# Kernel tuning notes

Hardware: AMD Instinct MI355X
Metric: run time of the kernel (lower is better)

The kernel has to match this reference:

```python
import jax, jax.numpy as jnp
import numpy as np

B, N, D = 128, 512, 128   # batch, nodes (= patch_len / time_window_size), feature dim (d_model_patch)
EPS = 1e-5                # torch BatchNorm1d default eps
SLOPE = 0.01              # torch F.leaky_relu default negative_slope
DIAG_INF = 1e8            # eyes_like * 100000000.0 in Dot_Graph_Construction_weights


def mask_matrix(T, decay):
    # Faithful replication of Mask_Matrix: slices i*T:(i+1)*T on a [T,T] array
    # are empty for i >= 1, so the result is all ones; we replicate exactly.
    A = np.ones((T, T), np.float32)
    for i in range(T):
        v = 0
        for r in range(i, T):
            A[i * T:(i + 1) * T, r * T:(r + 1) * T] *= decay ** v
            v += 1
        v = 0
        for r in range(i + 1):
            A[i * T:(i + 1) * T, (i - r) * T:(i - r + 1) * T] *= decay ** v
            v += 1
    return A


def setup_inputs() -> dict:
    key = jax.random.key(0)
    ks = jax.random.split(key, 3)
    s = 1.0 / np.sqrt(D)  # torch Linear default init scale
    return {
        "x": jax.random.normal(ks[0], (B, N, D), jnp.float32),
        "W_map": jax.random.uniform(ks[1], (D, D), jnp.float32, -s, s),
        "b_map": jnp.zeros((D,), jnp.float32),
        "W_theta": jax.random.uniform(ks[2], (D, D), jnp.float32, -s, s),
        "b_theta": jnp.zeros((D,), jnp.float32),
        "gamma_in": jnp.ones((D,), jnp.float32),
        "beta_in": jnp.zeros((D,), jnp.float32),
        "gamma_out": jnp.ones((D,), jnp.float32),
        "beta_out": jnp.zeros((D,), jnp.float32),
        "pre_relation": jnp.asarray(mask_matrix(N, 0.9)),
    }


def leaky_relu(x):
    return jnp.where(x >= 0, x, SLOPE * x)


def batchnorm(x, gamma, beta):
    # x: [B, N, C]; BatchNorm1d over channel C (training-mode batch stats,
    # matching torch transpose -> BN -> transpose pattern).
    mean = x.mean((0, 1))
    var = x.var((0, 1))
    return (x - mean) * jax.lax.rsqrt(var + EPS) * gamma + beta


def reference(x, W_map, b_map, W_theta, b_theta, gamma_in, beta_in,
              gamma_out, beta_out, pre_relation):
    # --- Dot_Graph_Construction_weights ---
    nf = x @ W_map + b_map                         # [B,N,D]
    adj = jnp.einsum('bnd,bmd->bnm', nf, nf)       # [B,N,N]
    eye = jnp.eye(N, dtype=x.dtype)
    adj = leaky_relu(adj - eye * DIAG_INF)
    adj = jax.nn.softmax(adj, axis=-1) + eye
    # --- decay mask (all-ones, computed faithfully) ---
    adj = adj * pre_relation
    # --- input BN ---
    xb = batchnorm(x, gamma_in, beta_in)
    # --- MPNN_mk_v2, k=1 ---
    h = jnp.einsum('bnm,bmd->bnd', adj, xb) @ W_theta + b_theta
    h = batchnorm(h, gamma_out, beta_out)
    return leaky_relu(h)                           # [B,N,D]
```

## Files before the change

### kernel.cpp

```cpp
#include <hip/hip_runtime.h>
#include <hip/hip_bf16.h>

#define B_ 128
#define N_ 512
#define D_ 128
#define M_ (B_ * N_)
#define LDSP 136

typedef unsigned short u16;
typedef short s8v __attribute__((ext_vector_type(8)));
typedef _Float16 h8v __attribute__((ext_vector_type(8)));
typedef __fp16 fp2v __attribute__((ext_vector_type(2)));
typedef float f4v __attribute__((ext_vector_type(4)));
typedef unsigned u4v __attribute__((ext_vector_type(4)));

__device__ __forceinline__ u16 f2h(float f) {
  _Float16 h = (_Float16)f;
  return __builtin_bit_cast(u16, h);
}
__device__ __forceinline__ float h2f(u16 v) {
  return (float)__builtin_bit_cast(_Float16, v);
}
__device__ __forceinline__ unsigned cvtpk_h(float a, float b) {
  fp2v r = __builtin_amdgcn_cvt_pkrtz(a, b);
  return __builtin_bit_cast(unsigned, r);
}
__device__ __forceinline__ u16* swzK(u16* base, int row, int col) {
  return (u16*)((char*)base + row * 256 + ((col * 2) ^ ((row & 15) << 4)));
}
__device__ __forceinline__ u16* swz64(u16* base, int row, int col) {
  return (u16*)((char*)base + row * 128 + ((col * 2) ^ ((row & 7) << 4)));
}
__device__ __forceinline__ int kperm(int c) {
  return (c & 3) + ((c >> 2) & 1) * 16 + ((c >> 3) & 3) * 4 + (c >> 5) * 32;
}
__device__ __forceinline__ void derive_ss(const float* __restrict__ stats,
                                          const float* __restrict__ gamma,
                                          const float* __restrict__ beta,
                                          float* sSS, int t) {
  if (t < 128) {
    float mean = stats[t] * (1.0f / (float)M_);
    float var  = stats[128 + t] * (1.0f / (float)M_) - mean * mean;
    float sc = gamma[t] * rsqrtf(var + 1e-5f);
    sSS[t] = sc;
    sSS[128 + t] = beta[t] - mean * sc;
  }
}
__device__ __forceinline__ void derive_ss8(const float* __restrict__ stats,
                                           const float* __restrict__ gamma,
                                           const float* __restrict__ beta,
                                           float* sSS, int t) {
  if (t < 128) {
    float sum = 0.f, sq = 0.f;
#pragma unroll
    for (int p = 0; p < 8; ++p) {
      sum += stats[p * 256 + t];
      sq  += stats[p * 256 + 128 + t];
    }
    float mean = sum * (1.0f / (float)M_);
    float var  = sq * (1.0f / (float)M_) - mean * mean;
    float sc = gamma[t] * rsqrtf(var + 1e-5f);
    sSS[t] = sc;
    sSS[128 + t] = beta[t] - mean * sc;
  }
}

__global__ __launch_bounds__(256) void prologue(const float* __restrict__ Wa,
                                                const float* __restrict__ Wb,
                                                u16* __restrict__ WT1,
                                                u16* __restrict__ WT2,
                                                const float* __restrict__ X,
                                                float* __restrict__ stats) {
  const int t = threadIdx.x;
  const int id = blockIdx.x;
  if (id < 128) {
    const float* W = (id < 64) ? Wa : Wb;
    u16* T = (id < 64) ? WT1 : WT2;
    const int idx = (id & 63) * 256 + t;
    const int k = idx >> 7, j = idx & 127;
    T[j * 128 + k] = f2h(W[idx]);
    return;
  }
  const int gid = id - 128;
  const int g = t & 31;
  const int h = t >> 5;
  const size_t r0 = (size_t)gid * 64;
  float s[4] = {0.f, 0.f, 0.f, 0.f}, q[4] = {0.f, 0.f, 0.f, 0.f};
#pragma unroll
  for (int r = h; r < 64; r += 8) {
    float4 v = *(const float4*)&X[(r0 + r) * D_ + g * 4];
    s[0] += v.x; q[0] += v.x * v.x;
    s[1] += v.y; q[1] += v.y * v.y;
    s[2] += v.z; q[2] += v.z * v.z;
    s[3] += v.w; q[3] += v.w * v.w;
  }
  __shared__ float red[256][8];
#pragma unroll
  for (int j = 0; j < 4; ++j) { red[t][j] = s[j]; red[t][4 + j] = q[j]; }
  __syncthreads();
  if (t < 32) {
    float S[4] = {0.f, 0.f, 0.f, 0.f}, Q[4] = {0.f, 0.f, 0.f, 0.f};
    for (int hh = 0; hh < 8; ++hh) {
      const float* p = red[hh * 32 + t];
#pragma unroll
      for (int j = 0; j < 4; ++j) { S[j] += p[j]; Q[j] += p[4 + j]; }
    }
    float* part = stats + (gid & 7) * 256;
#pragma unroll
    for (int j = 0; j < 4; ++j) {
      atomicAdd(&part[t * 4 + j], S[j]);
      atomicAdd(&part[128 + t * 4 + j], Q[j]);
    }
  }
}

__global__ __launch_bounds__(256) void xbT_kernel(const float* __restrict__ X,
                                                  const float* __restrict__ stats,
                                                  const float* __restrict__ gamma,
                                                  const float* __restrict__ beta,
                                                  u16* __restrict__ XBT) {
  __shared__ __align__(16) u16 sT[128][LDSP];
  __shared__ float sSS[256];
  const int t = threadIdx.x;
  const int b = blockIdx.x >> 2;
  const int n0 = (blockIdx.x & 3) * 128;
  const size_t xbase = (size_t)b * N_ * D_;
  const size_t tbase = (size_t)b * D_ * N_;
  derive_ss8(stats, gamma, beta, sSS, t);
  __syncthreads();
  {
    const int r = t >> 1, c0 = (t & 1) * 64;
#pragma unroll
    for (int i = 0; i < 16; ++i) {
      const int c = c0 + i * 4;
      float4 v = *(const float4*)&X[xbase + (size_t)(n0 + r) * D_ + c];
      sT[c + 0][r] = f2h(v.x * sSS[c + 0] + sSS[128 + c + 0]);
      sT[c + 1][r] = f2h(v.y * sSS[c + 1] + sSS[128 + c + 1]);
      sT[c + 2][r] = f2h(v.z * sSS[c + 2] + sSS[128 + c + 2]);
      sT[c + 3][r] = f2h(v.w * sSS[c + 3] + sSS[128 + c + 3]);
    }
  }
  __syncthreads();
  {
    const int d = t >> 1, nc = (t & 1) * 64;
#pragma unroll
    for (int i = 0; i < 8; ++i) {
      u16 o[8];
#pragma unroll
      for (int e = 0; e < 8; ++e) {
        const int L = nc + i * 8 + e;
        o[e] = sT[d][kperm(L & 63) + (L & 64)];
      }
      *(s8v*)&XBT[tbase + (size_t)d * N_ + n0 + nc + i * 8] = *(const s8v*)o;
    }
  }
}

__global__ __launch_bounds__(256, 2) void gemm1(const float* __restrict__ A,
                                                const u16* __restrict__ WT,
                                                const float* __restrict__ bias,
                                                u16* __restrict__ C) {
  __shared__ __align__(16) u16 sW[128][LDSP];
  const int t = threadIdx.x;
  const int wv = t >> 6, ln = t & 63, l16 = ln & 15, kg = ln >> 4;
  const size_t row0 = (size_t)blockIdx.x * 128;

#pragma unroll
  for (int i = 0; i < 8; ++i) {
    int o = t * 8 + i * 2048;
    *(s8v*)&sW[o >> 7][o & 127] = *(const s8v*)&WT[o];
  }

  h8v af[2][4];
#pragma unroll
  for (int rf = 0; rf < 2; ++rf) {
    const size_t row = row0 + wv * 32 + rf * 16 + l16;
#pragma unroll
    for (int kt = 0; kt < 4; ++kt) {
      const float* p = &A[row * D_ + kt * 32 + kg * 8];
      float4 v0 = *(const float4*)p;
      float4 v1 = *(const float4*)(p + 4);
      u16 hh[8];
      hh[0] = f2h(v0.x); hh[1] = f2h(v0.y); hh[2] = f2h(v0.z); hh[3] = f2h(v0.w);
      hh[4] = f2h(v1.x); hh[5] = f2h(v1.y); hh[6] = f2h(v1.z); hh[7] = f2h(v1.w);
      af[rf][kt] = *(const h8v*)hh;
    }
  }
  __syncthreads();

  f4v acc[2][8];
#pragma unroll
  for (int rf = 0; rf < 2; ++rf)
#pragma unroll
    for (int jf = 0; jf < 8; ++jf) acc[rf][jf] = f4v{0.f, 0.f, 0.f, 0.f};

#pragma unroll
  for (int kt = 0; kt < 4; ++kt) {
    const int k0 = kt * 32 + kg * 8;
#pragma unroll
    for (int jf = 0; jf < 8; ++jf) {
      h8v bw = *(const h8v*)&sW[jf * 16 + l16][k0];
      acc[0][jf] = __builtin_amdgcn_mfma_f32_16x16x32_f16(af[0][kt], bw, acc[0][jf], 0, 0, 0);
      acc[1][jf] = __builtin_amdgcn_mfma_f32_16x16x32_f16(af[1][kt], bw, acc[1][jf], 0, 0, 0);
    }
  }

#pragma unroll
  for (int rf = 0; rf < 2; ++rf) {
#pragma unroll
    for (int reg = 0; reg < 4; ++reg) {
      const int row = wv * 32 + rf * 16 + kg * 4 + reg;
#pragma unroll
      for (int jf = 0; jf < 8; ++jf) {
        const int col = jf * 16 + l16;
        C[(row0 + row) * D_ + col] = f2h(acc[rf][jf][reg] + bias[col]);
      }
    }
  }
}

__global__ __launch_bounds__(256, 2) void gemm2(const u16* __restrict__ A,
                                                const u16* __restrict__ WT,
                                                const float* __restrict__ bias,
                                                u16* __restrict__ C,
                                                float* __restrict__ stats) {
  __shared__ __align__(16) u16 sW[128][LDSP];
  __shared__ float sSum[128], sSq[128];
  const int t = threadIdx.x;
  const int wv = t >> 6, ln = t & 63, l16 = ln & 15, kg = ln >> 4;
  const size_t row0 = (size_t)blockIdx.x * 128;

  if (t < 128) { sSum[t] = 0.f; sSq[t] = 0.f; }
#pragma unroll
  for (int i = 0; i < 8; ++i) {
    int o = t * 8 + i * 2048;
    *(s8v*)&sW[o >> 7][o & 127] = *(const s8v*)&WT[o];
  }

  h8v a[2][4];
#pragma unroll
  for (int rf = 0; rf < 2; ++rf) {
    const size_t row = row0 + wv * 32 + rf * 16 + l16;
#pragma unroll
    for (int kt = 0; kt < 4; ++kt)
      a[rf][kt] = *(const h8v*)&A[row * D_ + kt * 32 + kg * 8];
  }
  __syncthreads();

  f4v acc[2][8];
#pragma unroll
  for (int rf = 0; rf < 2; ++rf)
#pragma unroll
    for (int jf = 0; jf < 8; ++jf) acc[rf][jf] = f4v{0.f, 0.f, 0.f, 0.f};

#pragma unroll
  for (int kt = 0; kt < 4; ++kt) {
    const int k0 = kt * 32 + kg * 8;
#pragma unroll
    for (int jf = 0; jf < 8; ++jf) {
      h8v bw = *(const h8v*)&sW[jf * 16 + l16][k0];
      acc[0][jf] = __builtin_amdgcn_mfma_f32_16x16x32_f16(a[0][kt], bw, acc[0][jf], 0, 0, 0);
      acc[1][jf] = __builtin_amdgcn_mfma_f32_16x16x32_f16(a[1][kt], bw, acc[1][jf], 0, 0, 0);
    }
  }

  float cs[8], cq[8];
#pragma unroll
  for (int jf = 0; jf < 8; ++jf) { cs[jf] = 0.f; cq[jf] = 0.f; }
#pragma unroll
  for (int rf = 0; rf < 2; ++rf) {
#pragma unroll
    for (int reg = 0; reg < 4; ++reg) {
      const int row = wv * 32 + rf * 16 + kg * 4 + reg;
#pragma unroll
      for (int jf = 0; jf < 8; ++jf) {
        const int col = jf * 16 + l16;
        u16 hb = f2h(acc[rf][jf][reg] + bias[col]);
        C[(row0 + row) * D_ + col] = hb;
        float vr = h2f(hb);
        cs[jf] += vr;
        cq[jf] += vr * vr;
      }
    }
  }
#pragma unroll
  for (int jf = 0; jf < 8; ++jf) {
    cs[jf] += __shfl_xor(cs[jf], 16); cq[jf] += __shfl_xor(cq[jf], 16);
    cs[jf] += __shfl_xor(cs[jf], 32); cq[jf] += __shfl_xor(cq[jf], 32);
  }
  if (kg == 0) {
#pragma unroll
    for (int jf = 0; jf < 8; ++jf) {
      atomicAdd(&sSum[jf * 16 + l16], cs[jf]);
      atomicAdd(&sSq[jf * 16 + l16], cq[jf]);
    }
  }
  __syncthreads();
  if (t < 128) {
    atomicAdd(&stats[t], sSum[t]);
    atomicAdd(&stats[128 + t], sSq[t]);
  }
}

__global__ __launch_bounds__(512, 4) void attn_kernel(const u16* __restrict__ NF,
                                                      const u16* __restrict__ XBT,
                                                      const float* __restrict__ X,
                                                      const float* __restrict__ stats,
                                                      const float* __restrict__ gamma,
                                                      const float* __restrict__ beta,
                                                      u16* __restrict__ ATT) {
  __shared__ __align__(16) u16 pool[17408];
  __shared__ float sSS[256];
  u16* sK  = pool;
  u16* sVT = pool + 8192;
  const int t = threadIdx.x;
  const int wv = t >> 6, ln = t & 63, l16 = ln & 15, kg = ln >> 4;
  const int id = blockIdx.x;
  const int b = (id & 7) + (id >> 5) * 8;
  const int r0 = ((id >> 3) & 3) * 128;
  const size_t base  = (size_t)b * N_ * D_;
  const size_t baseT = (size_t)b * D_ * N_;

  derive_ss8(stats, gamma, beta, sSS, t);

  h8v qf[4];
  {
    const size_t qoff = base + (size_t)(r0 + wv * 16 + l16) * D_ + kg * 8;
#pragma unroll
    for (int kt = 0; kt < 4; ++kt)
      qf[kt] = *(const h8v*)&NF[qoff + kt * 32];
  }

  const int kr = t >> 3, kc = (t & 7) * 16;
  const int vd = t >> 2, vc = (t & 3) * 16;
  const u16* gK = &NF[base + (size_t)kr * D_ + kc];
  const u16* gV = &XBT[baseT + (size_t)vd * N_ + vc];
  s8v rh0 = *(const s8v*)gK, rh1 = *(const s8v*)(gK + 8);
  s8v rv0 = *(const s8v*)gV, rv1 = *(const s8v*)(gV + 8);

  float m = -3e38f, l = 0.f;
  f4v accO[8];
#pragma unroll
  for (int df = 0; df < 8; ++df) accO[df] = f4v{0.f, 0.f, 0.f, 0.f};

  const int qg = r0 + wv * 16 + l16;
  const int qtile = qg & ~63;

  for (int j0 = 0; j0 < N_; j0 += 64) {
    *(s8v*)swzK(sK, kr, kc)       = rh0;
    *(s8v*)swzK(sK, kr, kc + 8)   = rh1;
    *(s8v*)swz64(sVT, vd, vc)     = rv0;
    *(s8v*)swz64(sVT, vd, vc + 8) = rv1;
    if (j0 + 64 < N_) {
      const int jn = j0 + 64;
      rh0 = *(const s8v*)(gK + (size_t)jn * D_);
      rh1 = *(const s8v*)(gK + (size_t)jn * D_ + 8);
      rv0 = *(const s8v*)(gV + jn);
      rv1 = *(const s8v*)(gV + jn + 8);
    }
    __syncthreads();

    f4v accS[4];
#pragma unroll
    for (int jf = 0; jf < 4; ++jf) accS[jf] = f4v{0.f, 0.f, 0.f, 0.f};
    __builtin_amdgcn_s_setprio(1);
#pragma unroll
    for (int kt = 0; kt < 4; ++kt) {
      const int k0 = kt * 32 + kg * 8;
#pragma unroll
      for (int jf = 0; jf < 4; ++jf) {
        h8v k_ = *(const h8v*)swzK(sK, jf * 16 + l16, k0);
        accS[jf] = __builtin_amdgcn_mfma_f32_16x16x32_f16(k_, qf[kt], accS[jf], 0, 0, 0);
      }
    }
    __builtin_amdgcn_s_setprio(0);

    float mx = -3e38f;
    if (j0 == qtile) {
#pragma unroll
      for (int jf = 0; jf < 4; ++jf) {
#pragma unroll
        for (int reg = 0; reg < 4; ++reg) {
          const int kk = j0 + jf * 16 + kg * 4 + reg;
          float sv = accS[jf][reg];
          if (kk == qg) sv -= 1e8f;
          sv = (sv >= 0.f) ? sv : 0.01f * sv;
          accS[jf][reg] = sv;
          mx = fmaxf(mx, sv);
        }
      }
    } else {
#pragma unroll
      for (int jf = 0; jf < 4; ++jf) {
#pragma unroll
        for (int reg = 0; reg < 4; ++reg) {
          float sv = accS[jf][reg];
          sv = (sv >= 0.f) ? sv : 0.01f * sv;
          accS[jf][reg] = sv;
          mx = fmaxf(mx, sv);
        }
      }
    }
    mx = fmaxf(mx, __shfl_xor(mx, 16));
    mx = fmaxf(mx, __shfl_xor(mx, 32));
    const bool resc = !__all(mx - m <= 8.0f);
    const float mnew = resc ? fmaxf(m, mx) : m;
    float rs = 0.f;
#pragma unroll
    for (int jf = 0; jf < 4; ++jf) {
#pragma unroll
      for (int reg = 0; reg < 4; ++reg) {
        const float p = __expf(accS[jf][reg] - mnew);
        accS[jf][reg] = p;
        rs += p;
      }
    }
    rs += __shfl_xor(rs, 16);
    rs += __shfl_xor(rs, 32);
    if (resc) {
      const float scl = __expf(m - mnew);
      l = l * scl + rs;
      m = mnew;
#pragma unroll
      for (int df = 0; df < 8; ++df) accO[df] = accO[df] * scl;
    } else {
      l += rs;
    }

    u4v w0, w1;
    w0[0] = cvtpk_h(accS[0][0], accS[0][1]);
    w0[1] = cvtpk_h(accS[0][2], accS[0][3]);
    w0[2] = cvtpk_h(accS[1][0], accS[1][1]);
    w0[3] = cvtpk_h(accS[1][2], accS[1][3]);
    w1[0] = cvtpk_h(accS[2][0], accS[2][1]);
    w1[1] = cvtpk_h(accS[2][2], accS[2][3]);
    w1[2] = cvtpk_h(accS[3][0], accS[3][1]);
    w1[3] = cvtpk_h(accS[3][2], accS[3][3]);
    h8v pb0, pb1;
    __builtin_memcpy(&pb0, &w0, 16);
    __builtin_memcpy(&pb1, &w1, 16);

    __builtin_amdgcn_s_setprio(1);
#pragma unroll
    for (int kt2 = 0; kt2 < 2; ++kt2) {
      const int k0 = kt2 * 32 + kg * 8;
      const h8v pb = kt2 ? pb1 : pb0;
#pragma unroll
      for (int df = 0; df < 8; ++df) {
        h8v av = *(const h8v*)swz64(sVT, df * 16 + l16, k0);
        accO[df] = __builtin_amdgcn_mfma_f32_16x16x32_f16(av, pb, accO[df], 0, 0, 0);
      }
    }
    __builtin_amdgcn_s_setprio(0);
    __syncthreads();
  }

  const float inv = 1.0f / l;
  u16* sOut = pool;
#pragma unroll
  for (int df = 0; df < 8; ++df) {
#pragma unroll
    for (int reg = 0; reg < 4; ++reg) {
      const int d = df * 16 + kg * 4 + reg;
      sOut[d * 136 + wv * 16 + l16] = f2h(accO[df][reg] * inv);
    }
  }
  __syncthreads();
  {
    const int q = t >> 2, c0 = (t & 3) * 32;
    const size_t orow = base + (size_t)(r0 + q) * D_;
#pragma unroll
    for (int i = 0; i < 4; ++i) {
      u16 o[8];
#pragma unroll
      for (int e = 0; e < 8; ++e) {
        const int d = c0 + i * 8 + e;
        const float ov = h2f(sOut[d * 136 + q]);
        const float xb = X[orow + d] * sSS[d] + sSS[128 + d];
        o[e] = f2h(ov + xb);
      }
      *(s8v*)&ATT[orow + c0 + i * 8] = *(const s8v*)o;
    }
  }
}

__global__ __launch_bounds__(256) void affine_out(const u16* __restrict__ H,
                                                  const float* __restrict__ stats,
                                                  const float* __restrict__ gamma,
                                                  const float* __restrict__ beta,
                                                  float* __restrict__ Y) {
  __shared__ float sSS[256];
  const int t = threadIdx.x;
  derive_ss(stats, gamma, beta, sSS, t);
  __syncthreads();
  const size_t idx = (size_t)blockIdx.x * 256 + t;
  const int c0 = (int)(idx & 15) * 8;
  s8v v = *(const s8v*)&H[idx * 8];
  float o[8];
#pragma unroll
  for (int e = 0; e < 8; ++e) {
    float x = h2f((u16)v[e]);
    float y = x * sSS[c0 + e] + sSS[128 + c0 + e];
    o[e] = (y >= 0.f) ? y : 0.01f * y;
  }
  *(float4*)&Y[idx * 8]     = make_float4(o[0], o[1], o[2], o[3]);
  *(float4*)&Y[idx * 8 + 4] = make_float4(o[4], o[5], o[6], o[7]);
}

extern "C" void kernel_launch(void* const* d_in, const int* in_sizes, int n_in,
                              void* d_out, int out_size, void* d_ws, size_t ws_size,
                              hipStream_t stream) {
  const float* x         = (const float*)d_in[0];
  const float* W_map     = (const float*)d_in[1];
  const float* b_map     = (const float*)d_in[2];
  const float* W_theta   = (const float*)d_in[3];
  const float* b_theta   = (const float*)d_in[4];
  const float* gamma_in  = (const float*)d_in[5];
  const float* beta_in   = (const float*)d_in[6];
  const float* gamma_out = (const float*)d_in[7];
  const float* beta_out  = (const float*)d_in[8];
  float* out = (float*)d_out;

  char* ws = (char*)d_ws;
  float* stats_x = (float*)ws;
  float* stats_h = (float*)(ws + 8192);
  u16* WT1 = (u16*)(ws + 9216);
  u16* WT2 = WT1 + 128 * 128;
  const size_t BUF = (size_t)M_ * D_;
  u16* nf = WT2 + 128 * 128;

  u16* xbT  = (u16*)d_out;
  u16* attO = (u16*)d_out + BUF;

  (void)hipMemsetAsync(ws, 0, 9216, stream);

  prologue<<<1152, 256, 0, stream>>>(W_map, W_theta, WT1, WT2, x, stats_x);
  gemm1<<<512, 256, 0, stream>>>(x, WT1, b_map, nf);
  xbT_kernel<<<512, 256, 0, stream>>>(x, stats_x, gamma_in, beta_in, xbT);
  attn_kernel<<<512, 512, 0, stream>>>(nf, xbT, x, stats_x, gamma_in, beta_in, attO);
  gemm2<<<512, 256, 0, stream>>>(attO, WT2, b_theta, nf, stats_h);
  affine_out<<<4096, 256, 0, stream>>>(nf, stats_h, gamma_out, beta_out, out);
}
```

Before: 128.2 us.

## Switch attention kernel to 32x32x16 MFMA tiles with 4-wave blocks

Rewrites the attention kernel so each wave owns 32 query rows and uses 32x32x16 f16 MFMA for both QK^T and PV, with blocks shrunk from 8 to 4 waves. Global-to-LDS staging is widened to four 16-byte chunks per thread, and the softmax reductions lose one shuffle stage. The kperm helper also gets a new bit mapping. The aim is fewer MFMA and LDS read instructions per unit of work and better operand reuse, at the cost of more accumulator registers per thread and fewer waves per block to hide latency.

```diff
diff --git a/kernel.cpp b/kernel.cpp
--- a/kernel.cpp
+++ b/kernel.cpp
@@ -12,6 +12,7 @@
 typedef _Float16 h8v __attribute__((ext_vector_type(8)));
 typedef __fp16 fp2v __attribute__((ext_vector_type(2)));
 typedef float f4v __attribute__((ext_vector_type(4)));
+typedef float f16v __attribute__((ext_vector_type(16)));
 typedef unsigned u4v __attribute__((ext_vector_type(4)));
 
 __device__ __forceinline__ u16 f2h(float f) {
@@ -31,8 +32,8 @@
 __device__ __forceinline__ u16* swz64(u16* base, int row, int col) {
   return (u16*)((char*)base + row * 128 + ((col * 2) ^ ((row & 7) << 4)));
 }
-__device__ __forceinline__ int kperm(int c) {
-  return (c & 3) + ((c >> 2) & 1) * 16 + ((c >> 3) & 3) * 4 + (c >> 5) * 32;
+__device__ __forceinline__ int kperm(int s) {
+  return (s & 48) | ((s & 4) << 1) | ((s >> 1) & 4) | (s & 3);
 }
 __device__ __forceinline__ void derive_ss(const float* __restrict__ stats,
                                           const float* __restrict__ gamma,
@@ -302,7 +303,7 @@
   }
 }
 
-__global__ __launch_bounds__(512, 4) void attn_kernel(const u16* __restrict__ NF,
+__global__ __launch_bounds__(256, 2) void attn_kernel(const u16* __restrict__ NF,
                                                       const u16* __restrict__ XBT,
                                                       const float* __restrict__ X,
                                                       const float* __restrict__ stats,
@@ -314,7 +315,7 @@
   u16* sK  = pool;
   u16* sVT = pool + 8192;
   const int t = threadIdx.x;
-  const int wv = t >> 6, ln = t & 63, l16 = ln & 15, kg = ln >> 4;
+  const int wv = t >> 6, ln = t & 63, l31 = ln & 31, hi = ln >> 5;
   const int id = blockIdx.x;
   const int b = (id & 7) + (id >> 5) * 8;
   const int r0 = ((id >> 3) & 3) * 128;
@@ -323,133 +324,140 @@
 
   derive_ss8(stats, gamma, beta, sSS, t);
 
-  h8v qf[4];
+  h8v qf[8];
   {
-    const size_t qoff = base + (size_t)(r0 + wv * 16 + l16) * D_ + kg * 8;
-#pragma unroll
-    for (int kt = 0; kt < 4; ++kt)
-      qf[kt] = *(const h8v*)&NF[qoff + kt * 32];
-  }
-
-  const int kr = t >> 3, kc = (t & 7) * 16;
-  const int vd = t >> 2, vc = (t & 3) * 16;
-  const u16* gK = &NF[base + (size_t)kr * D_ + kc];
-  const u16* gV = &XBT[baseT + (size_t)vd * N_ + vc];
-  s8v rh0 = *(const s8v*)gK, rh1 = *(const s8v*)(gK + 8);
-  s8v rv0 = *(const s8v*)gV, rv1 = *(const s8v*)(gV + 8);
+    const size_t qoff = base + (size_t)(r0 + wv * 32 + l31) * D_ + hi * 8;
+#pragma unroll
+    for (int ds = 0; ds < 8; ++ds)
+      qf[ds] = *(const h8v*)&NF[qoff + ds * 16];
+  }
+
+  const int kr = t >> 2, kcg = (t & 3) * 32;
+  const int vd = t >> 1, vcg = (t & 1) * 32;
+  const u16* gK = &NF[base + (size_t)kr * D_ + kcg];
+  const u16* gV = &XBT[baseT + (size_t)vd * N_ + vcg];
+  s8v rk[4], rv[4];
+#pragma unroll
+  for (int i = 0; i < 4; ++i) {
+    rk[i] = *(const s8v*)(gK + i * 8);
+    rv[i] = *(const s8v*)(gV + i * 8);
+  }
 
   float m = -3e38f, l = 0.f;
-  f4v accO[8];
-#pragma unroll
-  for (int df = 0; df < 8; ++df) accO[df] = f4v{0.f, 0.f, 0.f, 0.f};
-
-  const int qg = r0 + wv * 16 + l16;
-  const int qtile = qg & ~63;
+  f16v accO[4];
+#pragma unroll
+  for (int ds = 0; ds < 4; ++ds)
+#pragma unroll
+    for (int r = 0; r < 16; ++r) accO[ds][r] = 0.f;
+
+  const int qg = r0 + wv * 32 + l31;
+  const int qtile = (r0 + wv * 32) & ~63;
 
   for (int j0 = 0; j0 < N_; j0 += 64) {
-    *(s8v*)swzK(sK, kr, kc)       = rh0;
-    *(s8v*)swzK(sK, kr, kc + 8)   = rh1;
-    *(s8v*)swz64(sVT, vd, vc)     = rv0;
-    *(s8v*)swz64(sVT, vd, vc + 8) = rv1;
+#pragma unroll
+    for (int i = 0; i < 4; ++i) {
+      *(s8v*)swzK(sK, kr, kcg + i * 8)  = rk[i];
+      *(s8v*)swz64(sVT, vd, vcg + i * 8) = rv[i];
+    }
     if (j0 + 64 < N_) {
       const int jn = j0 + 64;
-      rh0 = *(const s8v*)(gK + (size_t)jn * D_);
-      rh1 = *(const s8v*)(gK + (size_t)jn * D_ + 8);
-      rv0 = *(const s8v*)(gV + jn);
-      rv1 = *(const s8v*)(gV + jn + 8);
+#pragma unroll
+      for (int i = 0; i < 4; ++i) {
+        rk[i] = *(const s8v*)(gK + (size_t)jn * D_ + i * 8);
+        rv[i] = *(const s8v*)(gV + jn + i * 8);
+      }
     }
     __syncthreads();
 
-    f4v accS[4];
-#pragma unroll
-    for (int jf = 0; jf < 4; ++jf) accS[jf] = f4v{0.f, 0.f, 0.f, 0.f};
+    f16v accS0, accS1;
+#pragma unroll
+    for (int r = 0; r < 16; ++r) { accS0[r] = 0.f; accS1[r] = 0.f; }
     __builtin_amdgcn_s_setprio(1);
 #pragma unroll
-    for (int kt = 0; kt < 4; ++kt) {
-      const int k0 = kt * 32 + kg * 8;
-#pragma unroll
-      for (int jf = 0; jf < 4; ++jf) {
-        h8v k_ = *(const h8v*)swzK(sK, jf * 16 + l16, k0);
-        accS[jf] = __builtin_amdgcn_mfma_f32_16x16x32_f16(k_, qf[kt], accS[jf], 0, 0, 0);
-      }
+    for (int ds = 0; ds < 8; ++ds) {
+      const int c0 = ds * 16 + hi * 8;
+      h8v k0_ = *(const h8v*)swzK(sK, l31, c0);
+      h8v k1_ = *(const h8v*)swzK(sK, 32 + l31, c0);
+      accS0 = __builtin_amdgcn_mfma_f32_32x32x16_f16(k0_, qf[ds], accS0, 0, 0, 0);
+      accS1 = __builtin_amdgcn_mfma_f32_32x32x16_f16(k1_, qf[ds], accS1, 0, 0, 0);
     }
     __builtin_amdgcn_s_setprio(0);
 
     float mx = -3e38f;
     if (j0 == qtile) {
 #pragma unroll
-      for (int jf = 0; jf < 4; ++jf) {
-#pragma unroll
-        for (int reg = 0; reg < 4; ++reg) {
-          const int kk = j0 + jf * 16 + kg * 4 + reg;
-          float sv = accS[jf][reg];
-          if (kk == qg) sv -= 1e8f;
-          sv = (sv >= 0.f) ? sv : 0.01f * sv;
-          accS[jf][reg] = sv;
-          mx = fmaxf(mx, sv);
-        }
+      for (int r = 0; r < 16; ++r) {
+        const int krow = (r & 3) + 8 * (r >> 2) + 4 * hi;
+        float sv = accS0[r];
+        if (j0 + krow == qg) sv -= 1e8f;
+        sv = (sv >= 0.f) ? sv : 0.01f * sv;
+        accS0[r] = sv; mx = fmaxf(mx, sv);
+        float sw = accS1[r];
+        if (j0 + 32 + krow == qg) sw -= 1e8f;
+        sw = (sw >= 0.f) ? sw : 0.01f * sw;
+        accS1[r] = sw; mx = fmaxf(mx, sw);
       }
     } else {
 #pragma unroll
-      for (int jf = 0; jf < 4; ++jf) {
-#pragma unroll
-        for (int reg = 0; reg < 4; ++reg) {
-          float sv = accS[jf][reg];
-          sv = (sv >= 0.f) ? sv : 0.01f * sv;
-          accS[jf][reg] = sv;
-          mx = fmaxf(mx, sv);
-        }
-      }
-    }
-    mx = fmaxf(mx, __shfl_xor(mx, 16));
+      for (int r = 0; r < 16; ++r) {
+        float sv = accS0[r];
+        sv = (sv >= 0.f) ? sv : 0.01f * sv;
+        accS0[r] = sv; mx = fmaxf(mx, sv);
+        float sw = accS1[r];
+        sw = (sw >= 0.f) ? sw : 0.01f * sw;
+        accS1[r] = sw; mx = fmaxf(mx, sw);
+      }
+    }
     mx = fmaxf(mx, __shfl_xor(mx, 32));
     const bool resc = !__all(mx - m <= 8.0f);
     const float mnew = resc ? fmaxf(m, mx) : m;
     float rs = 0.f;
 #pragma unroll
-    for (int jf = 0; jf < 4; ++jf) {
-#pragma unroll
-      for (int reg = 0; reg < 4; ++reg) {
-        const float p = __expf(accS[jf][reg] - mnew);
-        accS[jf][reg] = p;
-        rs += p;
-      }
-    }
-    rs += __shfl_xor(rs, 16);
+    for (int r = 0; r < 16; ++r) {
+      float p0 = __expf(accS0[r] - mnew);
+      float p1 = __expf(accS1[r] - mnew);
+      accS0[r] = p0; accS1[r] = p1;
+      rs += p0 + p1;
+    }
     rs += __shfl_xor(rs, 32);
     if (resc) {
       const float scl = __expf(m - mnew);
       l = l * scl + rs;
       m = mnew;
 #pragma unroll
-      for (int df = 0; df < 8; ++df) accO[df] = accO[df] * scl;
+      for (int ds = 0; ds < 4; ++ds)
+#pragma unroll
+        for (int r = 0; r < 16; ++r) accO[ds][r] *= scl;
     } else {
       l += rs;
     }
 
-    u4v w0, w1;
-    w0[0] = cvtpk_h(accS[0][0], accS[0][1]);
-    w0[1] = cvtpk_h(accS[0][2], accS[0][3]);
-    w0[2] = cvtpk_h(accS[1][0], accS[1][1]);
-    w0[3] = cvtpk_h(accS[1][2], accS[1][3]);
-    w1[0] = cvtpk_h(accS[2][0], accS[2][1]);
-    w1[1] = cvtpk_h(accS[2][2], accS[2][3]);
-    w1[2] = cvtpk_h(accS[3][0], accS[3][1]);
-    w1[3] = cvtpk_h(accS[3][2], accS[3][3]);
-    h8v pb0, pb1;
+    u4v w0, w1, w2, w3;
+#pragma unroll
+    for (int j = 0; j < 4; ++j) {
+      w0[j] = cvtpk_h(accS0[2 * j],     accS0[2 * j + 1]);
+      w1[j] = cvtpk_h(accS0[8 + 2 * j], accS0[9 + 2 * j]);
+      w2[j] = cvtpk_h(accS1[2 * j],     accS1[2 * j + 1]);
+      w3[j] = cvtpk_h(accS1[8 + 2 * j], accS1[9 + 2 * j]);
+    }
+    h8v pb0, pb1, pb2, pb3;
     __builtin_memcpy(&pb0, &w0, 16);
     __builtin_memcpy(&pb1, &w1, 16);
+    __builtin_memcpy(&pb2, &w2, 16);
+    __builtin_memcpy(&pb3, &w3, 16);
 
     __builtin_amdgcn_s_setprio(1);
 #pragma unroll
-    for (int kt2 = 0; kt2 < 2; ++kt2) {
-      const int k0 = kt2 * 32 + kg * 8;
-      const h8v pb = kt2 ? pb1 : pb0;
-#pragma unroll
-      for (int df = 0; df < 8; ++df) {
-        h8v av = *(const h8v*)swz64(sVT, df * 16 + l16, k0);
-        accO[df] = __builtin_amdgcn_mfma_f32_16x16x32_f16(av, pb, accO[df], 0, 0, 0);
-      }
+    for (int ds = 0; ds < 4; ++ds) {
+      const int row = ds * 32 + l31;
+      h8v av0 = *(const h8v*)swz64(sVT, row, 0 * 16 + hi * 8);
+      accO[ds] = __builtin_amdgcn_mfma_f32_32x32x16_f16(av0, pb0, accO[ds], 0, 0, 0);
+      h8v av1 = *(const h8v*)swz64(sVT, row, 1 * 16 + hi * 8);
+      accO[ds] = __builtin_amdgcn_mfma_f32_32x32x16_f16(av1, pb1, accO[ds], 0, 0, 0);
+      h8v av2 = *(const h8v*)swz64(sVT, row, 2 * 16 + hi * 8);
+      accO[ds] = __builtin_amdgcn_mfma_f32_32x32x16_f16(av2, pb2, accO[ds], 0, 0, 0);
+      h8v av3 = *(const h8v*)swz64(sVT, row, 3 * 16 + hi * 8);
+      accO[ds] = __builtin_amdgcn_mfma_f32_32x32x16_f16(av3, pb3, accO[ds], 0, 0, 0);
     }
     __builtin_amdgcn_s_setprio(0);
     __syncthreads();
@@ -458,19 +466,19 @@
   const float inv = 1.0f / l;
   u16* sOut = pool;
 #pragma unroll
-  for (int df = 0; df < 8; ++df) {
-#pragma unroll
-    for (int reg = 0; reg < 4; ++reg) {
-      const int d = df * 16 + kg * 4 + reg;
-      sOut[d * 136 + wv * 16 + l16] = f2h(accO[df][reg] * inv);
+  for (int ds = 0; ds < 4; ++ds) {
+#pragma unroll
+    for (int r = 0; r < 16; ++r) {
+      const int d = ds * 32 + (r & 3) + 8 * (r >> 2) + 4 * hi;
+      sOut[d * 136 + wv * 32 + l31] = f2h(accO[ds][r] * inv);
     }
   }
   __syncthreads();
   {
-    const int q = t >> 2, c0 = (t & 3) * 32;
+    const int q = t >> 1, c0 = (t & 1) * 64;
     const size_t orow = base + (size_t)(r0 + q) * D_;
 #pragma unroll
-    for (int i = 0; i < 4; ++i) {
+    for (int i = 0; i < 8; ++i) {
       u16 o[8];
 #pragma unroll
       for (int e = 0; e < 8; ++e) {
@@ -537,7 +545,7 @@
   prologue<<<1152, 256, 0, stream>>>(W_map, W_theta, WT1, WT2, x, stats_x);
   gemm1<<<512, 256, 0, stream>>>(x, WT1, b_map, nf);
   xbT_kernel<<<512, 256, 0, stream>>>(x, stats_x, gamma_in, beta_in, xbT);
-  attn_kernel<<<512, 512, 0, stream>>>(nf, xbT, x, stats_x, gamma_in, beta_in, attO);
+  attn_kernel<<<512, 256, 0, stream>>>(nf, xbT, x, stats_x, gamma_in, beta_in, attO);
   gemm2<<<512, 256, 0, stream>>>(attO, WT2, b_theta, nf, stats_h);
   affine_out<<<4096, 256, 0, stream>>>(nf, stats_h, gamma_out, beta_out, out);
 }
```

After: 127.8 us. Within noise of the previous version (-0.4%).
